# Kernel optimization log

Measured on AMD Instinct MI355X. Metric: run time of the kernel, lower is better.

Reference implementation:

```python
import jax, jax.numpy as jnp
import numpy as np

EPS = 1e-5


def _bn_eval(h, mean, var, gamma, beta):
    # BatchNorm1d in eval mode: normalize with running stats, then affine.
    return (h - mean) * (gamma / jnp.sqrt(var + EPS)) + beta


def setup_inputs() -> dict:
    key = jax.random.key(0)
    ks = jax.random.split(key, 17)
    B, D_IN, N_HEADS = 1024, 200, 128
    s = lambda k, shape, scale: jax.random.normal(k, shape, dtype=jnp.float32) * scale
    return {
        "x": s(ks[0], (B, D_IN), 1.0),
        # shared trunk
        "W0": s(ks[1], (D_IN, 2048), 1.0 / np.sqrt(D_IN)),
        "b0": s(ks[2], (2048,), 0.01),
        "g0": jax.random.uniform(ks[3], (2048,), dtype=jnp.float32, minval=0.5, maxval=1.5),
        "be0": s(ks[4], (2048,), 0.01),
        "m0": s(ks[5], (2048,), 0.1),
        "v0": jax.random.uniform(ks[6], (2048,), dtype=jnp.float32, minval=0.5, maxval=1.5),
        "W1": s(ks[7], (2048, 1024), 1.0 / np.sqrt(2048)),
        "b1": s(ks[8], (1024,), 0.01),
        "g1": jax.random.uniform(ks[9], (1024,), dtype=jnp.float32, minval=0.5, maxval=1.5),
        "be1": s(ks[10], (1024,), 0.01),
        "m1": s(ks[11], (1024,), 0.1),
        "v1": jax.random.uniform(ks[12], (1024,), dtype=jnp.float32, minval=0.5, maxval=1.5),
        # 128 parallel byte-predictor heads, stacked on axis 0
        "HW1": s(ks[13], (N_HEADS, 1024, 512), 1.0 / np.sqrt(1024)),
        "Hb1": s(ks[14], (N_HEADS, 512), 0.01),
        "HW2": s(ks[15], (N_HEADS, 512, 256), 1.0 / np.sqrt(512)),
        "Hb2": s(ks[16], (N_HEADS, 256), 0.01),
    }


def reference(x, W0, b0, g0, be0, m0, v0, W1, b1, g1, be1, m1, v1, HW1, Hb1, HW2, Hb2):
    # shared trunk: Linear -> BN -> ReLU -> (Dropout=id) -> Linear -> BN -> ReLU
    h = jax.nn.relu(_bn_eval(x @ W0 + b0, m0, v0, g0, be0))            # [B, 2048]
    feats = jax.nn.relu(_bn_eval(h @ W1 + b1, m1, v1, g1, be1))         # [B, 1024]
    # all 128 heads in one batched GEMM pair (equivalent to the per-head loop)
    z = jax.nn.relu(jnp.einsum('bd,ndh->bnh', feats, HW1) + Hb1)        # [B, 128, 512]
    out = jnp.einsum('bnh,nho->bno', z, HW2) + Hb2                      # [B, 128, 256]
    return out
```

## Files before the change

kernel.cpp:

```cpp
#include <hip/hip_runtime.h>
#include <hip/hip_bf16.h>
#include <stdint.h>


typedef __bf16 bf16x8 __attribute__((ext_vector_type(8)));
typedef float  floatx4 __attribute__((ext_vector_type(4)));
typedef unsigned short ushortx4 __attribute__((ext_vector_type(4)));
typedef unsigned short ushortx8 __attribute__((ext_vector_type(8)));

typedef __attribute__((address_space(1))) void as1_void;
typedef __attribute__((address_space(3))) void as3_void;

__device__ __forceinline__ void gld_lds16(const void* g, void* l) {
    __builtin_amdgcn_global_load_lds((as1_void*)g, (as3_void*)l, 16, 0, 0);
}

__device__ __forceinline__ unsigned short f2bf(float f) {
    __hip_bfloat16 h = __float2bfloat16(f);
    unsigned short s;
    __builtin_memcpy(&s, &h, 2);
    return s;
}

template <int MODE, typename OutT>
__global__ __launch_bounds__(256, 2)
void gemm_bt(const short* __restrict__ A, int lda, long aBatch,
             const short* __restrict__ B, int ldb, long bBatch,
             OutT* __restrict__ C, int ldc, long cBatch,
             int K, int ntilesN,
             const float* __restrict__ p0, const float* __restrict__ p1,
             const float* __restrict__ p2, const float* __restrict__ p3,
             const float* __restrict__ p4, int pBatch)
{
    __shared__ short As[128 * 32];
    __shared__ short Bs[128 * 32];

    const int tid  = threadIdx.x;
    const int w    = tid >> 6;
    const int l    = tid & 63;
    const int head = blockIdx.y;
    const int mt   = blockIdx.x / ntilesN;
    const int nt   = blockIdx.x % ntilesN;
    const int m0   = mt * 128;
    const int n0   = nt * 128;

    A += (long)head * aBatch;
    B += (long)head * bBatch;
    C += (long)head * cBatch;
    const float* pb = p0 + (long)head * pBatch;

    const int wm   = (w >> 1) * 64;
    const int wn   = (w & 1) * 64;
    const int lrow = l & 15;
    const int lk   = (l >> 4) * 8;

    floatx4 acc[4][4] = {};

    const int srow = l >> 2;
    const int scol = (l & 3) * 8;
    const short* Ag = A + (long)(m0 + w * 16 + srow) * lda + scol;
    const short* Bg = B + (long)(n0 + w * 16 + srow) * ldb + scol;
    const long a64 = (long)64 * lda;
    const long b64 = (long)64 * ldb;
    short* AsW0 = &As[(w * 16) * 32];
    short* AsW1 = &As[(64 + w * 16) * 32];
    short* BsW0 = &Bs[(w * 16) * 32];
    short* BsW1 = &Bs[(64 + w * 16) * 32];

    for (int k0 = 0; k0 < K; k0 += 32) {
        gld_lds16(Ag + k0,       AsW0);
        gld_lds16(Ag + a64 + k0, AsW1);
        gld_lds16(Bg + k0,       BsW0);
        gld_lds16(Bg + b64 + k0, BsW1);
        __syncthreads();

        bf16x8 af[4], bfr[4];
#pragma unroll
        for (int i = 0; i < 4; ++i)
            af[i] = *(const bf16x8*)&As[(wm + i * 16 + lrow) * 32 + lk];
#pragma unroll
        for (int j = 0; j < 4; ++j)
            bfr[j] = *(const bf16x8*)&Bs[(wn + j * 16 + lrow) * 32 + lk];

#pragma unroll
        for (int i = 0; i < 4; ++i)
#pragma unroll
            for (int j = 0; j < 4; ++j)
                acc[i][j] = __builtin_amdgcn_mfma_f32_16x16x32_bf16(
                    af[i], bfr[j], acc[i][j], 0, 0, 0);
        __syncthreads();
    }

    const int erow = (l >> 4) * 4;
    const int ecol = l & 15;
#pragma unroll
    for (int j = 0; j < 4; ++j) {
        const int nj = n0 + wn + j * 16 + ecol;
        float scale = 1.f, shift;
        if constexpr (MODE == 0) {
            const float s = p1[nj] * rsqrtf(p4[nj] + 1e-5f);
            scale = s;
            shift = (pb[nj] - p3[nj]) * s + p2[nj];
        } else {
            shift = pb[nj];
        }
#pragma unroll
        for (int i = 0; i < 4; ++i) {
            const long mi = m0 + wm + i * 16 + erow;
#pragma unroll
            for (int r = 0; r < 4; ++r) {
                float v = acc[i][j][r] * scale + shift;
                if constexpr (MODE != 2) v = fmaxf(v, 0.f);
                const long idx = (mi + r) * (long)ldc + nj;
                if constexpr (sizeof(OutT) == 2) C[idx] = (OutT)f2bf(v);
                else                             C[idx] = (OutT)v;
            }
        }
    }
}

__global__ __launch_bounds__(256)
void transpose64(const float* __restrict__ in, unsigned short* __restrict__ out,
                 int R, int C, long inBatch, long outBatch)
{
    __shared__ unsigned short lt[64 * 68];
    in  += (long)blockIdx.z * inBatch;
    out += (long)blockIdx.z * outBatch;
    const int c0 = blockIdx.x * 64;
    const int r0 = blockIdx.y * 64;
    const int t  = threadIdx.x;

    {
        const int rb = t >> 4;
        const int cg = (t & 15) * 4;
        floatx4 v[4];
#pragma unroll
        for (int i = 0; i < 4; ++i)
            v[i] = *(const floatx4*)&in[(long)(r0 + rb * 4 + i) * C + c0 + cg];
#pragma unroll
        for (int j = 0; j < 4; ++j) {
            ushortx4 col;
#pragma unroll
            for (int i = 0; i < 4; ++i) col[i] = f2bf(v[i][j]);
            *(ushortx4*)&lt[(cg + j) * 68 + rb * 4] = col;
        }
    }
    __syncthreads();

#pragma unroll
    for (int it = 0; it < 2; ++it) {
        const int idx = t + it * 256;
        const int c   = idx >> 3;
        const int rc  = idx & 7;
        ushortx4 lo = *(const ushortx4*)&lt[c * 68 + rc * 8];
        ushortx4 hi = *(const ushortx4*)&lt[c * 68 + rc * 8 + 4];
        ushortx8 o;
        o[0] = lo[0]; o[1] = lo[1]; o[2] = lo[2]; o[3] = lo[3];
        o[4] = hi[0]; o[5] = hi[1]; o[6] = hi[2]; o[7] = hi[3];
        *(ushortx8*)&out[(long)(c0 + c) * R + r0 + rc * 8] = o;
    }
}

__global__ void transpose_f32_bf16(const float* __restrict__ in, short* __restrict__ out,
                                   int R, int C, int Rpad, long inBatch, long outBatch)
{
    __shared__ float tile[32][33];
    in  += (long)blockIdx.z * inBatch;
    out += (long)blockIdx.z * outBatch;
    const int c0 = blockIdx.x * 32;
    const int r0 = blockIdx.y * 32;
    const int tx = threadIdx.x, ty = threadIdx.y;
#pragma unroll
    for (int rr = 0; rr < 4; ++rr) {
        const int r = r0 + ty + rr * 8;
        float v = 0.f;
        if (r < R) v = in[(long)r * C + c0 + tx];
        tile[ty + rr * 8][tx] = v;
    }
    __syncthreads();
#pragma unroll
    for (int rr = 0; rr < 4; ++rr) {
        const int oc = ty + rr * 8;
        out[(long)(c0 + oc) * Rpad + r0 + tx] = (short)f2bf(tile[tx][oc]);
    }
}

__global__ void pad_convert(const float* __restrict__ in, short* __restrict__ out,
                            int C, int Cpad, int total)
{
    const int idx = blockIdx.x * 256 + threadIdx.x;
    if (idx >= total) return;
    const int r = idx / Cpad, c = idx % Cpad;
    out[idx] = (short)f2bf(c < C ? in[(long)r * C + c] : 0.f);
}


extern "C" void kernel_launch(void* const* d_in, const int* in_sizes, int n_in,
                              void* d_out, int out_size, void* d_ws, size_t ws_size,
                              hipStream_t stream)
{
    const float* x   = (const float*)d_in[0];
    const float* W0  = (const float*)d_in[1];
    const float* b0  = (const float*)d_in[2];
    const float* g0  = (const float*)d_in[3];
    const float* be0 = (const float*)d_in[4];
    const float* m0  = (const float*)d_in[5];
    const float* v0  = (const float*)d_in[6];
    const float* W1  = (const float*)d_in[7];
    const float* b1  = (const float*)d_in[8];
    const float* g1  = (const float*)d_in[9];
    const float* be1 = (const float*)d_in[10];
    const float* m1  = (const float*)d_in[11];
    const float* v1  = (const float*)d_in[12];
    const float* HW1 = (const float*)d_in[13];
    const float* Hb1 = (const float*)d_in[14];
    const float* HW2 = (const float*)d_in[15];
    const float* Hb2 = (const float*)d_in[16];
    float* out = (float*)d_out;

    char* ws = (char*)d_ws;
    size_t off = 0;
    short* xb   = (short*)(ws + off); off += (size_t)1024 * 224 * 2;
    short* W0T  = (short*)(ws + off); off += (size_t)2048 * 224 * 2;
    short* W1T  = (short*)(ws + off); off += (size_t)1024 * 2048 * 2;
    short* HW1T = (short*)(ws + off); off += (size_t)128 * 512 * 1024 * 2;
    short* HW2T = (short*)(ws + off); off += (size_t)128 * 256 * 512 * 2;
    short* h    = (short*)(ws + off); off += (size_t)1024 * 2048 * 2;
    short* fts  = (short*)(ws + off); off += (size_t)1024 * 1024 * 2;
    short* z    = (short*)(ws + off); off += (size_t)1024 * 128 * 512 * 2;

    pad_convert<<<dim3((1024 * 224) / 256), dim3(256), 0, stream>>>(x, xb, 200, 224, 1024 * 224);
    transpose_f32_bf16<<<dim3(64, 7, 1), dim3(32, 8), 0, stream>>>(W0, W0T, 200, 2048, 224, 0, 0);
    transpose64<<<dim3(16, 32, 1), dim3(256), 0, stream>>>(
        W1, (unsigned short*)W1T, 2048, 1024, 0, 0);
    transpose64<<<dim3(8, 16, 128), dim3(256), 0, stream>>>(
        HW1, (unsigned short*)HW1T, 1024, 512, (long)1024 * 512, (long)512 * 1024);
    transpose64<<<dim3(4, 8, 128), dim3(256), 0, stream>>>(
        HW2, (unsigned short*)HW2T, 512, 256, (long)512 * 256, (long)256 * 512);

    gemm_bt<0, short><<<dim3(8 * 16, 1), dim3(256), 0, stream>>>(
        xb, 224, 0, W0T, 224, 0, h, 2048, 0, 224, 16, b0, g0, be0, m0, v0, 0);
    gemm_bt<0, short><<<dim3(8 * 8, 1), dim3(256), 0, stream>>>(
        h, 2048, 0, W1T, 2048, 0, fts, 1024, 0, 2048, 8, b1, g1, be1, m1, v1, 0);
    gemm_bt<1, short><<<dim3(8 * 4, 128), dim3(256), 0, stream>>>(
        fts, 1024, 0, HW1T, 1024, (long)512 * 1024, z, 128 * 512, 512,
        1024, 4, Hb1, nullptr, nullptr, nullptr, nullptr, 512);
    gemm_bt<2, float><<<dim3(8 * 2, 128), dim3(256), 0, stream>>>(
        z, 128 * 512, 512, HW2T, 512, (long)256 * 512, out, 128 * 256, 256,
        512, 2, Hb2, nullptr, nullptr, nullptr, nullptr, 256);

    (void)in_sizes; (void)n_in; (void)out_size; (void)ws_size;
}
```

Measured before the change: 811.2 us.

## Fuse the two per-head GEMMs into one kernel keeping z in LDS

```diff
diff --git a/kernel.cpp b/kernel.cpp
--- a/kernel.cpp
+++ b/kernel.cpp
@@ -22,15 +22,14 @@
     return s;
 }
 
-template <int MODE, typename OutT>
 __global__ __launch_bounds__(256, 2)
-void gemm_bt(const short* __restrict__ A, int lda, long aBatch,
-             const short* __restrict__ B, int ldb, long bBatch,
-             OutT* __restrict__ C, int ldc, long cBatch,
+void gemm_bt(const short* __restrict__ A, int lda,
+             const short* __restrict__ B, int ldb,
+             short* __restrict__ C, int ldc,
              int K, int ntilesN,
              const float* __restrict__ p0, const float* __restrict__ p1,
              const float* __restrict__ p2, const float* __restrict__ p3,
-             const float* __restrict__ p4, int pBatch)
+             const float* __restrict__ p4)
 {
     __shared__ short As[128 * 32];
     __shared__ short Bs[128 * 32];
@@ -38,16 +37,10 @@
     const int tid  = threadIdx.x;
     const int w    = tid >> 6;
     const int l    = tid & 63;
-    const int head = blockIdx.y;
     const int mt   = blockIdx.x / ntilesN;
     const int nt   = blockIdx.x % ntilesN;
     const int m0   = mt * 128;
     const int n0   = nt * 128;
-
-    A += (long)head * aBatch;
-    B += (long)head * bBatch;
-    C += (long)head * cBatch;
-    const float* pb = p0 + (long)head * pBatch;
 
     const int wm   = (w >> 1) * 64;
     const int wn   = (w & 1) * 64;
@@ -96,25 +89,136 @@
 #pragma unroll
     for (int j = 0; j < 4; ++j) {
         const int nj = n0 + wn + j * 16 + ecol;
-        float scale = 1.f, shift;
-        if constexpr (MODE == 0) {
-            const float s = p1[nj] * rsqrtf(p4[nj] + 1e-5f);
-            scale = s;
-            shift = (pb[nj] - p3[nj]) * s + p2[nj];
-        } else {
-            shift = pb[nj];
-        }
+        const float s = p1[nj] * rsqrtf(p4[nj] + 1e-5f);
+        const float shift = (p0[nj] - p3[nj]) * s + p2[nj];
 #pragma unroll
         for (int i = 0; i < 4; ++i) {
             const long mi = m0 + wm + i * 16 + erow;
 #pragma unroll
             for (int r = 0; r < 4; ++r) {
-                float v = acc[i][j][r] * scale + shift;
-                if constexpr (MODE != 2) v = fmaxf(v, 0.f);
-                const long idx = (mi + r) * (long)ldc + nj;
-                if constexpr (sizeof(OutT) == 2) C[idx] = (OutT)f2bf(v);
-                else                             C[idx] = (OutT)v;
+                float v = fmaxf(acc[i][j][r] * s + shift, 0.f);
+                C[(mi + r) * (long)ldc + nj] = (short)f2bf(v);
             }
+        }
+    }
+}
+
+__global__ __launch_bounds__(256, 3)
+void fused_heads(const short* __restrict__ feats,
+                 const short* __restrict__ HW1T,
+                 const short* __restrict__ HW2T,
+                 const float* __restrict__ Hb1,
+                 const float* __restrict__ Hb2,
+                 float* __restrict__ out)
+{
+    __shared__ short As[64 * 32];
+    __shared__ short Bs[128 * 32];
+    __shared__ short B2s[256 * 32];
+    __shared__ short zs[64 * 136];
+
+    const int tid  = threadIdx.x;
+    const int w    = tid >> 6;
+    const int l    = tid & 63;
+    const int mt   = blockIdx.x;
+    const int head = blockIdx.y;
+    const int m0   = mt * 64;
+
+    const int lrow = l & 15;
+    const int lk   = (l >> 4) * 8;
+    const int erow = (l >> 4) * 4;
+    const int ecol = l & 15;
+
+    const short* W1h = HW1T + (long)head * 512 * 1024;
+    const short* W2h = HW2T + (long)head * 256 * 512;
+
+    const int srow = l >> 2;
+    const int scol = (l & 3) * 8;
+
+    const short* AgBase  = feats + (long)(m0 + w * 16 + srow) * 1024 + scol;
+    short* AsW = &As[(w * 16) * 32];
+
+    floatx4 acc2[4][4] = {};
+
+    for (int c = 0; c < 4; ++c) {
+        floatx4 acc1[4][2] = {};
+        const short* BgBase = W1h + (long)(c * 128 + w * 16 + srow) * 1024 + scol;
+        short* BsW0 = &Bs[(w * 16) * 32];
+        short* BsW1 = &Bs[(64 + w * 16) * 32];
+
+        for (int k0 = 0; k0 < 1024; k0 += 32) {
+            gld_lds16(AgBase + k0,               AsW);
+            gld_lds16(BgBase + k0,               BsW0);
+            gld_lds16(BgBase + (long)64 * 1024 + k0, BsW1);
+            __syncthreads();
+
+            bf16x8 af[4], bfr[2];
+#pragma unroll
+            for (int i = 0; i < 4; ++i)
+                af[i] = *(const bf16x8*)&As[(i * 16 + lrow) * 32 + lk];
+#pragma unroll
+            for (int j = 0; j < 2; ++j)
+                bfr[j] = *(const bf16x8*)&Bs[(w * 32 + j * 16 + lrow) * 32 + lk];
+
+#pragma unroll
+            for (int i = 0; i < 4; ++i)
+#pragma unroll
+                for (int j = 0; j < 2; ++j)
+                    acc1[i][j] = __builtin_amdgcn_mfma_f32_16x16x32_bf16(
+                        af[i], bfr[j], acc1[i][j], 0, 0, 0);
+            __syncthreads();
+        }
+
+#pragma unroll
+        for (int j = 0; j < 2; ++j) {
+            const int kz = w * 32 + j * 16 + ecol;
+            const float bias = Hb1[head * 512 + c * 128 + kz];
+#pragma unroll
+            for (int i = 0; i < 4; ++i) {
+                const int mrow = i * 16 + erow;
+#pragma unroll
+                for (int r = 0; r < 4; ++r) {
+                    const float v = fmaxf(acc1[i][j][r] + bias, 0.f);
+                    zs[(mrow + r) * 136 + kz] = (short)f2bf(v);
+                }
+            }
+        }
+
+        for (int kk = 0; kk < 4; ++kk) {
+            const short* B2g = W2h + (long)(w * 16 + srow) * 512 + c * 128 + kk * 32 + scol;
+#pragma unroll
+            for (int q = 0; q < 4; ++q)
+                gld_lds16(B2g + (long)q * 64 * 512, &B2s[(q * 64 + w * 16) * 32]);
+            __syncthreads();
+
+            bf16x8 af2[4], bf2[4];
+#pragma unroll
+            for (int i = 0; i < 4; ++i)
+                af2[i] = *(const bf16x8*)&zs[(i * 16 + lrow) * 136 + kk * 32 + lk];
+#pragma unroll
+            for (int j = 0; j < 4; ++j)
+                bf2[j] = *(const bf16x8*)&B2s[(w * 64 + j * 16 + lrow) * 32 + lk];
+
+#pragma unroll
+            for (int i = 0; i < 4; ++i)
+#pragma unroll
+                for (int j = 0; j < 4; ++j)
+                    acc2[i][j] = __builtin_amdgcn_mfma_f32_16x16x32_bf16(
+                        af2[i], bf2[j], acc2[i][j], 0, 0, 0);
+            __syncthreads();
+        }
+    }
+
+#pragma unroll
+    for (int j = 0; j < 4; ++j) {
+        const int n2 = w * 64 + j * 16 + ecol;
+        const float bias = Hb2[head * 256 + n2];
+#pragma unroll
+        for (int i = 0; i < 4; ++i) {
+            const long mi = m0 + i * 16 + erow;
+#pragma unroll
+            for (int r = 0; r < 4; ++r)
+                out[(mi + r) * (long)(128 * 256) + head * 256 + n2] =
+                    acc2[i][j][r] + bias;
         }
     }
 }
@@ -227,7 +331,6 @@
     short* HW2T = (short*)(ws + off); off += (size_t)128 * 256 * 512 * 2;
     short* h    = (short*)(ws + off); off += (size_t)1024 * 2048 * 2;
     short* fts  = (short*)(ws + off); off += (size_t)1024 * 1024 * 2;
-    short* z    = (short*)(ws + off); off += (size_t)1024 * 128 * 512 * 2;
 
     pad_convert<<<dim3((1024 * 224) / 256), dim3(256), 0, stream>>>(x, xb, 200, 224, 1024 * 224);
     transpose_f32_bf16<<<dim3(64, 7, 1), dim3(32, 8), 0, stream>>>(W0, W0T, 200, 2048, 224, 0, 0);
@@ -238,16 +341,12 @@
     transpose64<<<dim3(4, 8, 128), dim3(256), 0, stream>>>(
         HW2, (unsigned short*)HW2T, 512, 256, (long)512 * 256, (long)256 * 512);
 
-    gemm_bt<0, short><<<dim3(8 * 16, 1), dim3(256), 0, stream>>>(
-        xb, 224, 0, W0T, 224, 0, h, 2048, 0, 224, 16, b0, g0, be0, m0, v0, 0);
-    gemm_bt<0, short><<<dim3(8 * 8, 1), dim3(256), 0, stream>>>(
-        h, 2048, 0, W1T, 2048, 0, fts, 1024, 0, 2048, 8, b1, g1, be1, m1, v1, 0);
-    gemm_bt<1, short><<<dim3(8 * 4, 128), dim3(256), 0, stream>>>(
-        fts, 1024, 0, HW1T, 1024, (long)512 * 1024, z, 128 * 512, 512,
-        1024, 4, Hb1, nullptr, nullptr, nullptr, nullptr, 512);
-    gemm_bt<2, float><<<dim3(8 * 2, 128), dim3(256), 0, stream>>>(
-        z, 128 * 512, 512, HW2T, 512, (long)256 * 512, out, 128 * 256, 256,
-        512, 2, Hb2, nullptr, nullptr, nullptr, nullptr, 256);
+    gemm_bt<<<dim3(8 * 16), dim3(256), 0, stream>>>(
+        xb, 224, W0T, 224, h, 2048, 224, 16, b0, g0, be0, m0, v0);
+    gemm_bt<<<dim3(8 * 8), dim3(256), 0, stream>>>(
+        h, 2048, W1T, 2048, fts, 1024, 2048, 8, b1, g1, be1, m1, v1);
+    fused_heads<<<dim3(16, 128), dim3(256), 0, stream>>>(
+        fts, HW1T, HW2T, Hb1, Hb2, out);
 
     (void)in_sizes; (void)n_in; (void)out_size; (void)ws_size;
 }
```

After: 957.6 us. 1.18x slower.
